# Performance work log

Measured on AMD Instinct MI355X. Metric: run time of the kernel, lower is better.

Reference implementation:

```python
import jax, jax.numpy as jnp
import numpy as np

SAME_RANGE = 0.2  # depth tolerance for averaging splats at the same target pixel


def setup_inputs() -> dict:
    key = jax.random.key(0)
    k1, k2, k3 = jax.random.split(key, 3)
    B, C, H, W = 8, 3, 512, 1024
    obj = jax.random.normal(k1, (B, C, H, W), dtype=jnp.float32)
    flow = jax.random.normal(k2, (B, 2, H, W), dtype=jnp.float32)
    depth = jax.random.uniform(k3, (B, 1, H, W), dtype=jnp.float32)
    return {"obj": obj, "flow": flow, "depth": depth}


def reference(obj, flow, depth):
    # Forward-warping splat with per-target-pixel depth (z-buffer) test.
    # For each source pixel: warp by flow, round to nearest target pixel,
    # keep/average contributions whose depth is within same_range of the
    # minimum depth landing on that target pixel.
    B, C, H, W = obj.shape
    # p0: meshgrid with indexing='xy' stacked as (x, y) channels
    gx = jnp.arange(W, dtype=jnp.float32)[None, :]  # [1, W]
    gy = jnp.arange(H, dtype=jnp.float32)[:, None]  # [H, 1]
    p1x = gx + flow[:, 0]  # [B, H, W]
    p1y = gy + flow[:, 1]
    safe_x = jnp.clip(p1x, 0.0, W - 1)
    safe_y = jnp.clip(p1y, 0.0, H - 1)
    xi = jnp.round(safe_x).astype(jnp.int32)
    yi = jnp.round(safe_y).astype(jnp.int32)
    # flat target index, batch-offset so one segment op covers all batches
    boff = (jnp.arange(B, dtype=jnp.int32) * (H * W))[:, None, None]
    idx = (boff + yi * W + xi).reshape(-1)          # [B*H*W]
    d = depth.reshape(-1)                           # [B*H*W] (depth has 1 channel)
    n_seg = B * H * W
    # z-buffer: per-target minimum depth among all splatted source pixels
    dlut = jax.ops.segment_min(d, idx, num_segments=n_seg)
    # contributions within same_range of the winner are averaged
    keep = (d <= dlut[idx] + SAME_RANGE).astype(obj.dtype)  # [B*H*W]
    vals = obj.transpose(0, 2, 3, 1).reshape(-1, C)         # [B*H*W, C]
    sums = jax.ops.segment_sum(vals * keep[:, None], idx, num_segments=n_seg)
    cnts = jax.ops.segment_sum(keep, idx, num_segments=n_seg)
    out = jnp.where(cnts[:, None] > 0, sums / jnp.maximum(cnts[:, None], 1.0), 0.0)
    return out.reshape(B, H, W, C).transpose(0, 3, 1, 2)
```

## Files before the change

### kernel.cpp

```cpp
#include <hip/hip_runtime.h>

#define BB 8
#define CC 3
#define HH 512
#define WW 1024
#define HW (HH * WW)
#define NTOT (BB * HW)
#define SAME_RANGE 0.2f

#define R 4
#define TX 32
#define TY 32
#define TT (TX * TY)
#define RX (TX + 2 * R)
#define RY (TY + 2 * R)
#define QX (RX / 4)
#define NSLOT (RY * QX)
#define SLOT_ITERS 2
#define CAP 16384
#define D_SENTINEL 0x7F7F7F7F

#define FP_BIAS  16.0f
#define FP_SCALE 524288.0f

__device__ __forceinline__ unsigned int fp_enc(float v) {
    return (unsigned int)__float2uint_rn((v + FP_BIAS) * FP_SCALE);
}

__global__ __launch_bounds__(256) void prep_kernel(
        const float* __restrict__ flow,
        const float* __restrict__ depth,
        const float* __restrict__ obj,
        int* __restrict__ counter,
        float* __restrict__ list) {
    int t = blockIdx.x * blockDim.x + threadIdx.x;
    int base = t << 2;
    int b = base >> 19;
    int rem = base & (HW - 1);
    int y = rem >> 10;
    int x = rem & (WW - 1);
    const float4 fx4 = *reinterpret_cast<const float4*>(flow + (size_t)(b * 2 + 0) * HW + rem);
    const float4 fy4 = *reinterpret_cast<const float4*>(flow + (size_t)(b * 2 + 1) * HW + rem);
    float fxa[4] = {fx4.x, fx4.y, fx4.z, fx4.w};
    float fya[4] = {fy4.x, fy4.y, fy4.z, fy4.w};
    float yf = (float)y;
    #pragma unroll
    for (int j = 0; j < 4; ++j) {
        float fx = fxa[j] + (float)(x + j);
        float fy = fya[j] + yf;
        fx = fminf(fmaxf(fx, 0.0f), (float)(WW - 1));
        fy = fminf(fmaxf(fy, 0.0f), (float)(HH - 1));
        int xi = (int)rintf(fx);
        int yi = (int)rintf(fy);
        int dx = xi - (x + j); if (dx < 0) dx = -dx;
        int dy = yi - y;       if (dy < 0) dy = -dy;
        if (dx > R || dy > R) {
            int srem = rem + j;
            int idx = b * HW + yi * WW + xi;
            int pos = atomicAdd(counter, 1);
            if (pos < CAP) {
                float* e = list + (size_t)pos * 8;
                e[0] = __int_as_float(idx);
                e[1] = depth[b * HW + srem];
                e[2] = obj[(b * CC + 0) * HW + srem];
                e[3] = obj[(b * CC + 1) * HW + srem];
                e[4] = obj[(b * CC + 2) * HW + srem];
            }
        }
    }
}

__global__ __launch_bounds__(256) void gather_kernel(
        const float* __restrict__ obj,
        const float* __restrict__ flow,
        const float* __restrict__ depth,
        const int* __restrict__ counter,
        const float* __restrict__ list,
        float* __restrict__ out) {
    __shared__ int s_dmin[TT];
    __shared__ unsigned long long s_p01[TT];
    __shared__ unsigned long long s_p2c[TT];

    int b = blockIdx.z;
    int tx0 = blockIdx.x * TX;
    int ty0 = blockIdx.y * TY;
    int tid = threadIdx.x;

    for (int i = tid; i < TT; i += 256) {
        s_dmin[i] = D_SENTINEL;
        s_p01[i] = 0ull;
        s_p2c[i] = 0ull;
    }
    __syncthreads();

    int   c_rem[SLOT_ITERS];
    int   c_tl[SLOT_ITERS][4];
    float c_d[SLOT_ITERS][4];

    #pragma unroll
    for (int it = 0; it < SLOT_ITERS; ++it) {
        int s = tid + it * 256;
        int remv = -1;
        int tl[4] = {-1, -1, -1, -1};
        float dv[4] = {0.0f, 0.0f, 0.0f, 0.0f};
        if (s < NSLOT) {
            int sy = s / QX;
            int sx4 = s - sy * QX;
            int gy = ty0 - R + sy;
            int gxb = tx0 - R + (sx4 << 2);
            if (gy >= 0 && gy < HH && gxb >= 0 && gxb < WW) {
                int rem = gy * WW + gxb;
                const float4 fx4 = *reinterpret_cast<const float4*>(flow + (size_t)(b * 2 + 0) * HW + rem);
                const float4 fy4 = *reinterpret_cast<const float4*>(flow + (size_t)(b * 2 + 1) * HW + rem);
                const float4 dd4 = *reinterpret_cast<const float4*>(depth + (size_t)b * HW + rem);
                float fxa[4] = {fx4.x, fx4.y, fx4.z, fx4.w};
                float fya[4] = {fy4.x, fy4.y, fy4.z, fy4.w};
                float dda[4] = {dd4.x, dd4.y, dd4.z, dd4.w};
                float gyf = (float)gy;
                remv = rem;
                #pragma unroll
                for (int j = 0; j < 4; ++j) {
                    int px = gxb + j;
                    float fx = fxa[j] + (float)px;
                    float fy = fya[j] + gyf;
                    fx = fminf(fmaxf(fx, 0.0f), (float)(WW - 1));
                    fy = fminf(fmaxf(fy, 0.0f), (float)(HH - 1));
                    int xi = (int)rintf(fx);
                    int yi = (int)rintf(fy);
                    int ddx = xi - px; if (ddx < 0) ddx = -ddx;
                    int ddy = yi - gy; if (ddy < 0) ddy = -ddy;
                    if (ddx <= R && ddy <= R) {
                        int lx = xi - tx0;
                        int ly = yi - ty0;
                        if (lx >= 0 && lx < TX && ly >= 0 && ly < TY) {
                            int tloc = ly * TX + lx;
                            tl[j] = tloc;
                            dv[j] = dda[j];
                            atomicMin(&s_dmin[tloc], __float_as_int(dda[j]));
                        }
                    }
                }
            }
        }
        c_rem[it] = remv;
        #pragma unroll
        for (int j = 0; j < 4; ++j) { c_tl[it][j] = tl[j]; c_d[it][j] = dv[j]; }
    }

    int noutl = *counter;
    if (noutl > CAP) noutl = CAP;
    for (int j = tid; j < noutl; j += 256) {
        const float* e = list + (size_t)j * 8;
        int idx = __float_as_int(e[0]);
        if ((idx >> 19) == b) {
            int remt = idx & (HW - 1);
            int lx = (remt & (WW - 1)) - tx0;
            int ly = (remt >> 10) - ty0;
            if (lx >= 0 && lx < TX && ly >= 0 && ly < TY)
                atomicMin(&s_dmin[ly * TX + lx], __float_as_int(e[1]));
        }
    }
    __syncthreads();

    #pragma unroll
    for (int it = 0; it < SLOT_ITERS; ++it) {
        int rem = c_rem[it];
        if (rem >= 0) {
            const float4 o04 = *reinterpret_cast<const float4*>(obj + (size_t)(b * CC + 0) * HW + rem);
            const float4 o14 = *reinterpret_cast<const float4*>(obj + (size_t)(b * CC + 1) * HW + rem);
            const float4 o24 = *reinterpret_cast<const float4*>(obj + (size_t)(b * CC + 2) * HW + rem);
            float o0a[4] = {o04.x, o04.y, o04.z, o04.w};
            float o1a[4] = {o14.x, o14.y, o14.z, o14.w};
            float o2a[4] = {o24.x, o24.y, o24.z, o24.w};
            #pragma unroll
            for (int j = 0; j < 4; ++j) {
                int t = c_tl[it][j];
                if (t >= 0) {
                    float thresh = __int_as_float(s_dmin[t]) + SAME_RANGE;
                    if (c_d[it][j] <= thresh) {
                        unsigned long long p01 =
                            (unsigned long long)fp_enc(o0a[j]) |
                            ((unsigned long long)fp_enc(o1a[j]) << 32);
                        unsigned long long p2c =
                            (unsigned long long)fp_enc(o2a[j]) | (1ull << 32);
                        atomicAdd(&s_p01[t], p01);
                        atomicAdd(&s_p2c[t], p2c);
                    }
                }
            }
        }
    }
    for (int j = tid; j < noutl; j += 256) {
        const float* e = list + (size_t)j * 8;
        int idx = __float_as_int(e[0]);
        if ((idx >> 19) == b) {
            int remt = idx & (HW - 1);
            int lx = (remt & (WW - 1)) - tx0;
            int ly = (remt >> 10) - ty0;
            if (lx >= 0 && lx < TX && ly >= 0 && ly < TY) {
                int t = ly * TX + lx;
                float thresh = __int_as_float(s_dmin[t]) + SAME_RANGE;
                if (e[1] <= thresh) {
                    unsigned long long p01 =
                        (unsigned long long)fp_enc(e[2]) |
                        ((unsigned long long)fp_enc(e[3]) << 32);
                    unsigned long long p2c =
                        (unsigned long long)fp_enc(e[4]) | (1ull << 32);
                    atomicAdd(&s_p01[t], p01);
                    atomicAdd(&s_p2c[t], p2c);
                }
            }
        }
    }
    __syncthreads();

    for (int i = tid; i < TT; i += 256) {
        int lx = i & (TX - 1);
        int ly = i >> 5;
        int orem = (ty0 + ly) * WW + (tx0 + lx);
        unsigned long long p01 = s_p01[i];
        unsigned long long p2c = s_p2c[i];
        unsigned int cnt = (unsigned int)(p2c >> 32);
        float r0 = 0.0f, r1 = 0.0f, r2 = 0.0f;
        if (cnt > 0) {
            double inv = 1.0 / ((double)FP_SCALE * (double)cnt);
            r0 = (float)((double)(unsigned int)(p01 & 0xffffffffu) * inv - (double)FP_BIAS);
            r1 = (float)((double)(unsigned int)(p01 >> 32)         * inv - (double)FP_BIAS);
            r2 = (float)((double)(unsigned int)(p2c & 0xffffffffu) * inv - (double)FP_BIAS);
        }
        out[(b * CC + 0) * HW + orem] = r0;
        out[(b * CC + 1) * HW + orem] = r1;
        out[(b * CC + 2) * HW + orem] = r2;
    }
}

extern "C" void kernel_launch(void* const* d_in, const int* in_sizes, int n_in,
                              void* d_out, int out_size, void* d_ws, size_t ws_size,
                              hipStream_t stream) {
    const float* obj   = (const float*)d_in[0];
    const float* flow  = (const float*)d_in[1];
    const float* depth = (const float*)d_in[2];
    float* out = (float*)d_out;

    int*   counter = (int*)d_ws;
    float* list    = (float*)((char*)d_ws + 256);

    hipMemsetAsync(counter, 0, sizeof(int), stream);

    prep_kernel<<<dim3(NTOT / 1024), dim3(256), 0, stream>>>(
        flow, depth, obj, counter, list);

    gather_kernel<<<dim3(WW / TX, HH / TY, BB), dim3(256), 0, stream>>>(
        obj, flow, depth, counter, list, out);
}
```

Measured before the change: 165.5 us.

## Drop prep pass; collect far splats in gather and resolve them in fixup kernel

Removes the separate full-image prep kernel. The gather kernel now records splats that move farther than the halo radius into a global list, doing so only for source pixels inside its own tile so each is recorded once. It no longer scans that list in every block. A small fixup kernel then recomputes each listed target pixel from its 9x9 source neighbourhood plus the list entries and overwrites the output. The change also remaps block indices to interleave batches across workgroups. The cost is that in-tile near contributions and far contributions are combined in the fixup, which assumes the list stays small.

Result: faster. 153.1 us (-7.5%).

```diff
diff --git a/kernel.cpp b/kernel.cpp
--- a/kernel.cpp
+++ b/kernel.cpp
@@ -27,63 +27,23 @@
     return (unsigned int)__float2uint_rn((v + FP_BIAS) * FP_SCALE);
 }
 
-__global__ __launch_bounds__(256) void prep_kernel(
-        const float* __restrict__ flow,
-        const float* __restrict__ depth,
-        const float* __restrict__ obj,
-        int* __restrict__ counter,
-        float* __restrict__ list) {
-    int t = blockIdx.x * blockDim.x + threadIdx.x;
-    int base = t << 2;
-    int b = base >> 19;
-    int rem = base & (HW - 1);
-    int y = rem >> 10;
-    int x = rem & (WW - 1);
-    const float4 fx4 = *reinterpret_cast<const float4*>(flow + (size_t)(b * 2 + 0) * HW + rem);
-    const float4 fy4 = *reinterpret_cast<const float4*>(flow + (size_t)(b * 2 + 1) * HW + rem);
-    float fxa[4] = {fx4.x, fx4.y, fx4.z, fx4.w};
-    float fya[4] = {fy4.x, fy4.y, fy4.z, fy4.w};
-    float yf = (float)y;
-    #pragma unroll
-    for (int j = 0; j < 4; ++j) {
-        float fx = fxa[j] + (float)(x + j);
-        float fy = fya[j] + yf;
-        fx = fminf(fmaxf(fx, 0.0f), (float)(WW - 1));
-        fy = fminf(fmaxf(fy, 0.0f), (float)(HH - 1));
-        int xi = (int)rintf(fx);
-        int yi = (int)rintf(fy);
-        int dx = xi - (x + j); if (dx < 0) dx = -dx;
-        int dy = yi - y;       if (dy < 0) dy = -dy;
-        if (dx > R || dy > R) {
-            int srem = rem + j;
-            int idx = b * HW + yi * WW + xi;
-            int pos = atomicAdd(counter, 1);
-            if (pos < CAP) {
-                float* e = list + (size_t)pos * 8;
-                e[0] = __int_as_float(idx);
-                e[1] = depth[b * HW + srem];
-                e[2] = obj[(b * CC + 0) * HW + srem];
-                e[3] = obj[(b * CC + 1) * HW + srem];
-                e[4] = obj[(b * CC + 2) * HW + srem];
-            }
-        }
-    }
-}
-
 __global__ __launch_bounds__(256) void gather_kernel(
         const float* __restrict__ obj,
         const float* __restrict__ flow,
         const float* __restrict__ depth,
-        const int* __restrict__ counter,
-        const float* __restrict__ list,
+        int* __restrict__ counter,
+        float* __restrict__ list,
         float* __restrict__ out) {
     __shared__ int s_dmin[TT];
     __shared__ unsigned long long s_p01[TT];
     __shared__ unsigned long long s_p2c[TT];
 
-    int b = blockIdx.z;
-    int tx0 = blockIdx.x * TX;
-    int ty0 = blockIdx.y * TY;
+    int lin = blockIdx.x + 32 * blockIdx.y + 512 * blockIdx.z;
+    int wgid = (lin & 7) * 512 + (lin >> 3);
+    int b   = wgid >> 9;
+    int rr  = wgid & 511;
+    int tx0 = (rr & 31) * TX;
+    int ty0 = (rr >> 5) * TY;
     int tid = threadIdx.x;
 
     for (int i = tid; i < TT; i += 256) {
@@ -138,6 +98,18 @@
                             dv[j] = dda[j];
                             atomicMin(&s_dmin[tloc], __float_as_int(dda[j]));
                         }
+                    } else if (px >= tx0 && px < tx0 + TX &&
+                               gy >= ty0 && gy < ty0 + TY) {
+                        int srem = rem + j;
+                        int pos = atomicAdd(counter, 1);
+                        if (pos < CAP) {
+                            float* e = list + (size_t)pos * 8;
+                            e[0] = __int_as_float(b * HW + yi * WW + xi);
+                            e[1] = dda[j];
+                            e[2] = obj[(b * CC + 0) * HW + srem];
+                            e[3] = obj[(b * CC + 1) * HW + srem];
+                            e[4] = obj[(b * CC + 2) * HW + srem];
+                        }
                     }
                 }
             }
@@ -145,20 +117,6 @@
         c_rem[it] = remv;
         #pragma unroll
         for (int j = 0; j < 4; ++j) { c_tl[it][j] = tl[j]; c_d[it][j] = dv[j]; }
-    }
-
-    int noutl = *counter;
-    if (noutl > CAP) noutl = CAP;
-    for (int j = tid; j < noutl; j += 256) {
-        const float* e = list + (size_t)j * 8;
-        int idx = __float_as_int(e[0]);
-        if ((idx >> 19) == b) {
-            int remt = idx & (HW - 1);
-            int lx = (remt & (WW - 1)) - tx0;
-            int ly = (remt >> 10) - ty0;
-            if (lx >= 0 && lx < TX && ly >= 0 && ly < TY)
-                atomicMin(&s_dmin[ly * TX + lx], __float_as_int(e[1]));
-        }
     }
     __syncthreads();
 
@@ -190,28 +148,6 @@
             }
         }
     }
-    for (int j = tid; j < noutl; j += 256) {
-        const float* e = list + (size_t)j * 8;
-        int idx = __float_as_int(e[0]);
-        if ((idx >> 19) == b) {
-            int remt = idx & (HW - 1);
-            int lx = (remt & (WW - 1)) - tx0;
-            int ly = (remt >> 10) - ty0;
-            if (lx >= 0 && lx < TX && ly >= 0 && ly < TY) {
-                int t = ly * TX + lx;
-                float thresh = __int_as_float(s_dmin[t]) + SAME_RANGE;
-                if (e[1] <= thresh) {
-                    unsigned long long p01 =
-                        (unsigned long long)fp_enc(e[2]) |
-                        ((unsigned long long)fp_enc(e[3]) << 32);
-                    unsigned long long p2c =
-                        (unsigned long long)fp_enc(e[4]) | (1ull << 32);
-                    atomicAdd(&s_p01[t], p01);
-                    atomicAdd(&s_p2c[t], p2c);
-                }
-            }
-        }
-    }
     __syncthreads();
 
     for (int i = tid; i < TT; i += 256) {
@@ -234,6 +170,85 @@
     }
 }
 
+__global__ __launch_bounds__(64) void fixup_kernel(
+        const float* __restrict__ obj,
+        const float* __restrict__ flow,
+        const float* __restrict__ depth,
+        const int* __restrict__ counter,
+        const float* __restrict__ list,
+        float* __restrict__ out) {
+    int noutl = *counter;
+    if (noutl > CAP) noutl = CAP;
+    int lane = threadIdx.x;
+    for (int o = blockIdx.x; o < noutl; o += gridDim.x) {
+        int tidx = __float_as_int(list[(size_t)o * 8]);
+        int tb   = tidx >> 19;
+        int trem = tidx & (HW - 1);
+        int tyy  = trem >> 10;
+        int txx  = trem & (WW - 1);
+        float cd[2] = {0.0f, 0.0f};
+        int   cr[2] = {-1, -1};
+        float dmin = 1e30f;
+        #pragma unroll
+        for (int c = 0; c < 2; ++c) {
+            int k = lane + c * 64;
+            if (k < 81) {
+                int ky = k / 9;
+                int sy = tyy - R + ky;
+                int sx = txx - R + (k - ky * 9);
+                if (sx >= 0 && sx < WW && sy >= 0 && sy < HH) {
+                    int srem = sy * WW + sx;
+                    float fx = flow[(tb * 2 + 0) * HW + srem] + (float)sx;
+                    float fy = flow[(tb * 2 + 1) * HW + srem] + (float)sy;
+                    fx = fminf(fmaxf(fx, 0.0f), (float)(WW - 1));
+                    fy = fminf(fmaxf(fy, 0.0f), (float)(HH - 1));
+                    if ((int)rintf(fx) == txx && (int)rintf(fy) == tyy) {
+                        float d = depth[tb * HW + srem];
+                        cd[c] = d; cr[c] = srem;
+                        dmin = fminf(dmin, d);
+                    }
+                }
+            }
+        }
+        for (int k = lane; k < noutl; k += 64) {
+            const float* e = list + (size_t)k * 8;
+            if (__float_as_int(e[0]) == tidx) dmin = fminf(dmin, e[1]);
+        }
+        #pragma unroll
+        for (int m = 32; m >= 1; m >>= 1)
+            dmin = fminf(dmin, __shfl_xor(dmin, m));
+        float thr = dmin + SAME_RANGE;
+        float s0 = 0.0f, s1 = 0.0f, s2 = 0.0f, cnt = 0.0f;
+        #pragma unroll
+        for (int c = 0; c < 2; ++c) {
+            if (cr[c] >= 0 && cd[c] <= thr) {
+                s0 += obj[(tb * CC + 0) * HW + cr[c]];
+                s1 += obj[(tb * CC + 1) * HW + cr[c]];
+                s2 += obj[(tb * CC + 2) * HW + cr[c]];
+                cnt += 1.0f;
+            }
+        }
+        for (int k = lane; k < noutl; k += 64) {
+            const float* e = list + (size_t)k * 8;
+            if (__float_as_int(e[0]) == tidx && e[1] <= thr) {
+                s0 += e[2]; s1 += e[3]; s2 += e[4]; cnt += 1.0f;
+            }
+        }
+        #pragma unroll
+        for (int m = 32; m >= 1; m >>= 1) {
+            s0  += __shfl_xor(s0, m);
+            s1  += __shfl_xor(s1, m);
+            s2  += __shfl_xor(s2, m);
+            cnt += __shfl_xor(cnt, m);
+        }
+        if (lane == 0) {
+            out[(tb * CC + 0) * HW + trem] = s0 / cnt;
+            out[(tb * CC + 1) * HW + trem] = s1 / cnt;
+            out[(tb * CC + 2) * HW + trem] = s2 / cnt;
+        }
+    }
+}
+
 extern "C" void kernel_launch(void* const* d_in, const int* in_sizes, int n_in,
                               void* d_out, int out_size, void* d_ws, size_t ws_size,
                               hipStream_t stream) {
@@ -247,9 +262,9 @@
 
     hipMemsetAsync(counter, 0, sizeof(int), stream);
 
-    prep_kernel<<<dim3(NTOT / 1024), dim3(256), 0, stream>>>(
-        flow, depth, obj, counter, list);
-
     gather_kernel<<<dim3(WW / TX, HH / TY, BB), dim3(256), 0, stream>>>(
         obj, flow, depth, counter, list, out);
-}
+
+    fixup_kernel<<<dim3(64), dim3(64), 0, stream>>>(
+        obj, flow, depth, counter, list, out);
+}
```
